# Kernel tuning notes

Measured on AMD Instinct MI355X. Metric: run time of the kernel, lower is better.

The kernel has to match this reference:

```python
import jax, jax.numpy as jnp
import numpy as np

BN_EPS = 1e-5
L2_EPS = 1e-12
TEMP = 0.01


def _fc(x, W, b, gamma, beta, mean, var, normalize):
    # Linear -> ReLU -> BatchNorm1d (eval mode, running stats) [-> L2 normalize]
    y = jnp.maximum(x @ W.T + b, 0.0)
    y = gamma * (y - mean) * jax.lax.rsqrt(var + BN_EPS) + beta
    if normalize:
        n = jnp.linalg.norm(y, axis=-1, keepdims=True)
        y = y / jnp.maximum(n, L2_EPS)
    return y


def setup_inputs() -> dict:
    key = jax.random.key(0)
    B, n, m = 8, 64, 2048
    inp_d0, con_d0, d1, d2, K = 1024, 2048, 2048, 2048, 7
    ks = jax.random.split(key, 16)
    s = 0.02
    inp = {
        'x': jax.random.normal(ks[0], (B, n, inp_d0, K, K), jnp.float32),
        'x_context': jax.random.normal(ks[1], (B, m, con_d0), jnp.float32),
        'num_valid_context_items': jax.random.randint(ks[2], (B, 1), 1, m + 1, jnp.int32),
        'q_W': jax.random.normal(ks[3], (d1, inp_d0)) * s,
        'q_b': jnp.zeros((d1,)),
        'q_gamma': jnp.ones((d1,)),
        'q_beta': jnp.zeros((d1,)),
        'q_mean': jax.random.normal(ks[4], (d1,)) * s,
        'q_var': jax.random.uniform(ks[5], (d1,), minval=0.5, maxval=1.5),
        'k_W': jax.random.normal(ks[6], (d1, con_d0)) * s,
        'k_b': jnp.zeros((d1,)),
        'k_gamma': jnp.ones((d1,)),
        'k_beta': jnp.zeros((d1,)),
        'k_mean': jax.random.normal(ks[7], (d1,)) * s,
        'k_var': jax.random.uniform(ks[8], (d1,), minval=0.5, maxval=1.5),
        'v_W': jax.random.normal(ks[9], (d2, con_d0)) * s,
        'v_b': jnp.zeros((d2,)),
        'v_gamma': jnp.ones((d2,)),
        'v_beta': jnp.zeros((d2,)),
        'v_mean': jax.random.normal(ks[10], (d2,)) * s,
        'v_var': jax.random.uniform(ks[11], (d2,), minval=0.5, maxval=1.5),
        'f_W': jax.random.normal(ks[12], (inp_d0, d2)) * s,
        'f_b': jnp.zeros((inp_d0,)),
        'f_gamma': jnp.ones((inp_d0,)),
        'f_beta': jnp.zeros((inp_d0,)),
        'f_mean': jax.random.normal(ks[13], (inp_d0,)) * s,
        'f_var': jax.random.uniform(ks[14], (inp_d0,), minval=0.5, maxval=1.5),
    }
    return inp


def reference(x, x_context, num_valid_context_items,
              q_W, q_b, q_gamma, q_beta, q_mean, q_var,
              k_W, k_b, k_gamma, k_beta, k_mean, k_var,
              v_W, v_b, v_gamma, v_beta, v_mean, v_var,
              f_W, f_b, f_gamma, f_beta, f_mean, f_var):
    # x: [B, n, D, K, K]; x_context: [B, m, C]; num_valid: [B, 1]
    A_pool = x.mean(axis=(-2, -1))                                  # [B, n, D]
    queries = _fc(A_pool, q_W, q_b, q_gamma, q_beta, q_mean, q_var, True)   # [B, n, d1]
    keys = _fc(x_context, k_W, k_b, k_gamma, k_beta, k_mean, k_var, True)   # [B, m, d1]
    values = _fc(x_context, v_W, v_b, v_gamma, v_beta, v_mean, v_var, True) # [B, m, d2]
    weights = jnp.einsum('bnd,bmd->bnm', queries, keys)             # [B, n, m]
    m = keys.shape[1]
    valid = jnp.arange(m)[None, :] < num_valid_context_items        # [B, m] bool
    weights = jnp.where(valid[:, None, :], weights, -jnp.inf)
    values = values * valid[:, :, None]
    weights = jax.nn.softmax(weights / TEMP, axis=-1)
    wv = jnp.einsum('bnm,bmd->bnd', weights, values)                # [B, n, d2]
    f_context = _fc(wv, f_W, f_b, f_gamma, f_beta, f_mean, f_var, False)    # [B, n, D]
    return x + f_context[..., None, None]
```

## Files before the change

kernel.cpp:

```cpp
#include <hip/hip_runtime.h>

typedef _Float16 f16;
typedef _Float16 f16x8 __attribute__((ext_vector_type(8)));
typedef _Float16 f16x4 __attribute__((ext_vector_type(4)));
typedef float f32x4 __attribute__((ext_vector_type(4)));
typedef float fv4 __attribute__((ext_vector_type(4)));

#define BN_EPS 1e-5f

constexpr int EPI_RAW = 0;
constexpr int EPI_HALF_NORM = 2;
constexpr int EPI_HALF = 3;
constexpr int EPI_BN_F32 = 4;
constexpr int EPI_HALF_NORM_T = 5;

__device__ __forceinline__ void gload_lds16(const void* g, void* l) {
  __builtin_amdgcn_global_load_lds(
      (const __attribute__((address_space(1))) unsigned int*)g,
      (__attribute__((address_space(3))) unsigned int*)l, 16, 0, 0);
}

template <int EPI>
__global__ __launch_bounds__(512, 1) void gemm8_kernel(
    const f16* __restrict__ A, const f16* __restrict__ Bh, int N, int K,
    int gx, f16* __restrict__ Ch, const float* __restrict__ bias,
    const float* __restrict__ gamma, const float* __restrict__ beta,
    const float* __restrict__ mean, const float* __restrict__ var,
    float* __restrict__ norm2) {
  __shared__ __align__(16) char smem[131072];

  const int nwg = gridDim.x;
  const int bid = blockIdx.x;
  const int swz = (bid & 7) * (nwg >> 3) + (bid >> 3);
  const int brow = (swz / gx) * 256;
  const int bcol = (swz % gx) * 256;

  const int tid = threadIdx.x;
  const int lane = tid & 63;
  const int w = tid >> 6;
  const int wm = w >> 2;
  const int wn = w & 3;
  const int l15 = lane & 15;
  const int l4 = lane >> 4;

  const int NT = K >> 6;

  const int c0 = tid ^ ((tid >> 3) & 3);
  const int srow = c0 >> 2;
  const int sk = (c0 & 3) * 8;
  const size_t gA0 = (size_t)(brow + srow) * K + sk;
  const size_t gB0 = (size_t)(bcol + srow) * K + sk;
  const size_t gstep = (size_t)128 * K;
  char* const ldst = smem + tid * 16;

  auto STAGE = [&](int v, int par, int op, int kk) {
    if (v >= NT) return;
    const int k0 = v * 64 + kk * 32;
    const f16* g = (op == 0) ? (A + gA0 + k0) : (Bh + gB0 + k0);
    char* l = ldst + par * 65536 + op * 32768 + kk * 16384;
    gload_lds16(g, l);
    gload_lds16(g + gstep, l + 8192);
  };

  f32x4 acc[8][4] = {};
  f16x8 fb[4];

  const int kx16 = (l4 ^ ((l15 >> 1) & 3)) * 16;
  const int aoff = ((wm * 128 + l15) << 6) + kx16;
  const int boff = 32768 + ((wn * 64 + l15) << 6) + kx16;

  auto ldf = [&](int off) -> f16x8 { return *(const f16x8*)(smem + off); };

  auto PH = [&](int par, int kk, int mi0, bool ldB, int sv, int spar, int sop,
                int skk, int wmode, int tcur, bool bar) {
    const int abase = par * 65536 + kk * 16384;
    if (ldB) {
#pragma unroll
      for (int ni = 0; ni < 4; ++ni) fb[ni] = ldf(abase + boff + (ni << 10));
    }
    f16x8 fa[4];
#pragma unroll
    for (int r = 0; r < 4; ++r) fa[r] = ldf(abase + aoff + ((mi0 + r) << 10));
    STAGE(sv, spar, sop, skk);
    __builtin_amdgcn_s_setprio(1);
#pragma unroll
    for (int r = 0; r < 4; ++r)
#pragma unroll
      for (int ni = 0; ni < 4; ++ni)
        acc[mi0 + r][ni] = __builtin_amdgcn_mfma_f32_16x16x32_f16(
            fa[r], fb[ni], acc[mi0 + r][ni], 0, 0, 0);
    __builtin_amdgcn_s_setprio(0);
    if (wmode == 1) {
      if (tcur + 2 >= NT)
        asm volatile("s_waitcnt vmcnt(0)" ::: "memory");
      else
        asm volatile("s_waitcnt vmcnt(4)" ::: "memory");
    } else if (wmode == 2) {
      if (tcur + 2 < NT) asm volatile("s_waitcnt vmcnt(4)" ::: "memory");
    }
    if (bar) __builtin_amdgcn_s_barrier();
  };

  STAGE(0, 0, 0, 0);
  STAGE(0, 0, 1, 0);
  STAGE(0, 0, 0, 1);
  STAGE(0, 0, 1, 1);
  STAGE(1, 1, 0, 0);
  STAGE(1, 1, 1, 0);
  asm volatile("s_waitcnt vmcnt(4)" ::: "memory");
  __builtin_amdgcn_s_barrier();

  for (int t = 0; t < NT; t += 2) {
    PH(0, 0, 0, true, t + 1, 1, 0, 1, 0, t, false);
    PH(0, 0, 4, false, t + 1, 1, 1, 1, 0, t, true);
    PH(0, 1, 0, true, t + 2, 0, 0, 0, 0, t, false);
    PH(0, 1, 4, false, t + 2, 0, 1, 0, 1, t, true);
    PH(1, 0, 0, true, t + 2, 0, 0, 1, 0, t, false);
    PH(1, 0, 4, false, t + 2, 0, 1, 1, 0, t, true);
    PH(1, 1, 0, true, t + 3, 1, 0, 0, 0, t, false);
    PH(1, 1, 4, false, t + 3, 1, 1, 0, 2, t, true);
  }

  if constexpr (EPI == EPI_HALF_NORM_T) {
    float colsum[4] = {0.f, 0.f, 0.f, 0.f};
#pragma unroll
    for (int mi = 0; mi < 8; ++mi) {
#pragma unroll
      for (int jj = 0; jj < 4; ++jj) {
        const int grow = brow + wm * 128 + mi * 16 + l4 * 4 + jj;
        const float bb = bias[grow], gg = gamma[grow], mm = mean[grow];
        const float vv = var[grow], be = beta[grow];
#pragma unroll
        for (int ni = 0; ni < 4; ++ni) {
          const int gcol = bcol + wn * 64 + ni * 16 + l15;
          float y = fmaxf(acc[mi][ni][jj] + bb, 0.0f);
          y = gg * (y - mm) / sqrtf(vv + BN_EPS) + be;
          Ch[(size_t)grow * N + gcol] = (f16)y;
          colsum[ni] += y * y;
        }
      }
    }
#pragma unroll
    for (int ni = 0; ni < 4; ++ni) {
      float s = colsum[ni];
      s += __shfl_xor(s, 16);
      s += __shfl_xor(s, 32);
      if (l4 == 0)
        atomicAdd(&norm2[bcol + wn * 64 + ni * 16 + l15], s);
    }
  } else {
#pragma unroll
    for (int mi = 0; mi < 8; ++mi) {
#pragma unroll
      for (int jj = 0; jj < 4; ++jj) {
        const int grow = brow + wm * 128 + mi * 16 + l4 * 4 + jj;
        float nsum = 0.0f;
#pragma unroll
        for (int ni = 0; ni < 4; ++ni) {
          const int gcol = bcol + wn * 64 + ni * 16 + l15;
          float y = fmaxf(acc[mi][ni][jj] + bias[gcol], 0.0f);
          y = gamma[gcol] * (y - mean[gcol]) / sqrtf(var[gcol] + BN_EPS) +
              beta[gcol];
          Ch[(size_t)grow * N + gcol] = (f16)y;
          nsum += y * y;
        }
        nsum += __shfl_xor(nsum, 1);
        nsum += __shfl_xor(nsum, 2);
        nsum += __shfl_xor(nsum, 4);
        nsum += __shfl_xor(nsum, 8);
        if (l15 == 0) atomicAdd(&norm2[grow], nsum);
      }
    }
  }
}

template <int BM, int BN, int EPI>
__global__ __launch_bounds__(256, 2) void gemm_kernel(
    const f16* __restrict__ Ah, const f16* __restrict__ Bh, int M, int N,
    int K, long long sAb, long long sBb, long long sCb,
    float* __restrict__ Cf, f16* __restrict__ Ch,
    const float* __restrict__ bias, const float* __restrict__ gamma,
    const float* __restrict__ beta, const float* __restrict__ mean,
    const float* __restrict__ var, float* __restrict__ norm2) {
  (void)M;
  constexpr int BK = 32;
  constexpr int WM = BM / 2, WN = BN / 2;
  constexpr int FM = WM / 16, FN = WN / 16;

  __shared__ __align__(16) f16 lds[(BM + BN) * BK];
  f16* sA = lds;
  f16* sB = lds + BM * BK;

  const int b = blockIdx.z;
  const f16* pA = Ah + (size_t)b * sAb;
  const f16* pB = Bh + (size_t)b * sBb;

  const int brow = blockIdx.y * BM, bcol = blockIdx.x * BN;
  const int t = threadIdx.x, wave = t >> 6, lane = t & 63;
  const int wr = wave >> 1, wc = wave & 1;

  f32x4 acc[FM][FN] = {};

  constexpr int A_CH = BM / 16, B_CH = BN / 16;
  constexpr int TOT = A_CH + B_CH;

  const int srow = lane >> 2;
  const int scol = (lane & 3) * 8;
  const int lr = lane & 15;
  const int lkb = (lane >> 4) * 8;

  for (int k0 = 0; k0 < K; k0 += BK) {
    for (int id = wave; id < TOT; id += 4) {
      const f16* g;
      f16* l;
      if (id < A_CH) {
        g = pA + (size_t)(brow + id * 16 + srow) * K + k0 + scol;
        l = sA + id * 16 * BK;
      } else {
        int c = id - A_CH;
        g = pB + (size_t)(bcol + c * 16 + srow) * K + k0 + scol;
        l = sB + c * 16 * BK;
      }
      gload_lds16(g, l);
    }
    asm volatile("s_waitcnt vmcnt(0)" ::: "memory");
    __syncthreads();

    f16x8 fa[FM], fb[FN];
#pragma unroll
    for (int mi = 0; mi < FM; ++mi)
      fa[mi] = *(const f16x8*)(sA + (size_t)(wr * WM + mi * 16 + lr) * BK + lkb);
#pragma unroll
    for (int ni = 0; ni < FN; ++ni)
      fb[ni] = *(const f16x8*)(sB + (size_t)(wc * WN + ni * 16 + lr) * BK + lkb);
#pragma unroll
    for (int mi = 0; mi < FM; ++mi)
#pragma unroll
      for (int ni = 0; ni < FN; ++ni)
        acc[mi][ni] = __builtin_amdgcn_mfma_f32_16x16x32_f16(fa[mi], fb[ni],
                                                             acc[mi][ni], 0, 0, 0);
    __syncthreads();
  }

#pragma unroll
  for (int mi = 0; mi < FM; ++mi) {
#pragma unroll
    for (int j = 0; j < 4; ++j) {
      const int grow = brow + wr * WM + mi * 16 + (lane >> 4) * 4 + j;
      float nsum = 0.0f;
#pragma unroll
      for (int ni = 0; ni < FN; ++ni) {
        const int gcol = bcol + wc * WN + ni * 16 + lr;
        float val = acc[mi][ni][j];
        if constexpr (EPI == EPI_RAW) {
          Cf[(size_t)b * sCb + (size_t)grow * N + gcol] = val;
        } else if constexpr (EPI == EPI_HALF) {
          Ch[(size_t)b * sCb + (size_t)grow * N + gcol] = (f16)val;
        } else {
          float y = fmaxf(val + bias[gcol], 0.0f);
          y = gamma[gcol] * (y - mean[gcol]) / sqrtf(var[gcol] + BN_EPS) +
              beta[gcol];
          if constexpr (EPI == EPI_BN_F32) {
            Cf[(size_t)grow * N + gcol] = y;
          } else {
            Ch[(size_t)grow * N + gcol] = (f16)y;
            nsum += y * y;
          }
        }
      }
      if constexpr (EPI == EPI_HALF_NORM) {
        nsum += __shfl_xor(nsum, 1);
        nsum += __shfl_xor(nsum, 2);
        nsum += __shfl_xor(nsum, 4);
        nsum += __shfl_xor(nsum, 8);
        if (lr == 0) atomicAdd(&norm2[grow], nsum);
      }
    }
  }
}

__global__ __launch_bounds__(256) void cvt_multi_kernel(
    const float* __restrict__ s0, f16* __restrict__ d0,
    const float* __restrict__ s1, f16* __restrict__ d1,
    const float* __restrict__ s2, f16* __restrict__ d2,
    const float* __restrict__ s3, f16* __restrict__ d3,
    const float* __restrict__ s4, f16* __restrict__ d4, int c0, int c1,
    int c2, int c3, int c4) {
  int i = blockIdx.x * 256 + threadIdx.x;
  if (i >= c4) return;
  const float* s;
  f16* d;
  int j;
  if (i < c0) {
    s = s0; d = d0; j = i;
  } else if (i < c1) {
    s = s1; d = d1; j = i - c0;
  } else if (i < c2) {
    s = s2; d = d2; j = i - c1;
  } else if (i < c3) {
    s = s3; d = d3; j = i - c2;
  } else {
    s = s4; d = d4; j = i - c3;
  }
  fv4 v = ((const fv4*)s)[j];
  f16x4 h;
#pragma unroll
  for (int k = 0; k < 4; ++k) h[k] = (f16)v[k];
  ((f16x4*)d)[j] = h;
}

__global__ __launch_bounds__(256) void pool_kernel(const float* __restrict__ x,
                                                   f16* __restrict__ ah) {
  int bn = blockIdx.x;
  const float* base = x + (size_t)bn * 1024 * 49;
  for (int d = threadIdx.x; d < 1024; d += 256) {
    const float* p = base + (size_t)d * 49;
    float s = 0.f;
#pragma unroll
    for (int j = 0; j < 49; ++j) s += p[j];
    ah[(size_t)bn * 1024 + d] = (f16)(s / 49.0f);
  }
}

__global__ __launch_bounds__(256) void softmax_kernel(
    const float* __restrict__ raw, const float* __restrict__ qn2,
    const float* __restrict__ kn2, const float* __restrict__ vn2,
    const int* __restrict__ nvalid, f16* __restrict__ wgt) {
  const int n = blockIdx.x;
  const int b = blockIdx.y;
  const int row = b * 64 + n;
  const float* r = raw + (size_t)row * 2048;
  const int nv = nvalid[b];
  const float qs = 100.0f / fmaxf(sqrtf(qn2[row]), 1e-12f);

  __shared__ float sl[2048];
  __shared__ float red[4];
  const int t = threadIdx.x;

  float mx = -3.0e38f;
  for (int m = t; m < 2048; m += 256) {
    float v = -3.0e38f;
    if (m < nv) {
      float ks = 1.0f / fmaxf(sqrtf(kn2[b * 2048 + m]), 1e-12f);
      v = r[m] * qs * ks;
    }
    sl[m] = v;
    mx = fmaxf(mx, v);
  }
#pragma unroll
  for (int s = 32; s; s >>= 1) mx = fmaxf(mx, __shfl_xor(mx, s));
  if ((t & 63) == 0) red[t >> 6] = mx;
  __syncthreads();
  mx = fmaxf(fmaxf(red[0], red[1]), fmaxf(red[2], red[3]));
  __syncthreads();

  float sum = 0.f;
  for (int m = t; m < 2048; m += 256) {
    float e = (m < nv) ? __expf(sl[m] - mx) : 0.0f;
    sl[m] = e;
    sum += e;
  }
#pragma unroll
  for (int s = 32; s; s >>= 1) sum += __shfl_xor(sum, s);
  if ((t & 63) == 0) red[t >> 6] = sum;
  __syncthreads();
  sum = red[0] + red[1] + red[2] + red[3];
  const float inv = 1.0f / sum;

  for (int m = t; m < 2048; m += 256) {
    float vs = 1.0f / fmaxf(sqrtf(vn2[b * 2048 + m]), 1e-12f);
    wgt[(size_t)row * 2048 + m] = (f16)(sl[m] * inv * vs);
  }
}

__global__ __launch_bounds__(256) void add_kernel(const float* __restrict__ x,
                                                  const float* __restrict__ fc,
                                                  float* __restrict__ out,
                                                  int n4) {
  int i = blockIdx.x * 256 + threadIdx.x;
  if (i >= n4) return;
  fv4 v = ((const fv4*)x)[i];
  int e = i * 4;
#pragma unroll
  for (int j = 0; j < 4; ++j) v[j] += fc[(e + j) / 49];
  ((fv4*)out)[i] = v;
}

extern "C" void kernel_launch(void* const* d_in, const int* in_sizes, int n_in,
                              void* d_out, int out_size, void* d_ws,
                              size_t ws_size, hipStream_t stream) {
  (void)in_sizes; (void)n_in; (void)out_size; (void)ws_size;
  const float* x = (const float*)d_in[0];
  const float* xc = (const float*)d_in[1];
  const int* nvp = (const int*)d_in[2];
  const float* qW = (const float*)d_in[3];
  const float* qB = (const float*)d_in[4];
  const float* qG = (const float*)d_in[5];
  const float* qBe = (const float*)d_in[6];
  const float* qM = (const float*)d_in[7];
  const float* qV = (const float*)d_in[8];
  const float* kW = (const float*)d_in[9];
  const float* kB = (const float*)d_in[10];
  const float* kG = (const float*)d_in[11];
  const float* kBe = (const float*)d_in[12];
  const float* kM = (const float*)d_in[13];
  const float* kV = (const float*)d_in[14];
  const float* vW = (const float*)d_in[15];
  const float* vB = (const float*)d_in[16];
  const float* vG = (const float*)d_in[17];
  const float* vBe = (const float*)d_in[18];
  const float* vM = (const float*)d_in[19];
  const float* vV = (const float*)d_in[20];
  const float* fW = (const float*)d_in[21];
  const float* fB = (const float*)d_in[22];
  const float* fG = (const float*)d_in[23];
  const float* fBe = (const float*)d_in[24];
  const float* fM = (const float*)d_in[25];
  const float* fV = (const float*)d_in[26];
  float* out = (float*)d_out;

  const int NRq = 512;
  const int NRc = 16384;
  const int Dd = 1024, Cc = 2048, D1 = 2048, D2 = 2048, Mm = 2048;

  char* p = (char*)d_ws;
  auto take = [&](size_t bytes) -> char* {
    char* r = p;
    p += (bytes + 255) & ~(size_t)255;
    return r;
  };
  f16* xch = (f16*)take((size_t)NRc * Cc * 2);
  f16* kh = (f16*)take((size_t)NRc * D1 * 2);
  f16* vT = (f16*)take((size_t)NRc * D2 * 2);
  f16* qWh = (f16*)take((size_t)D1 * Dd * 2);
  f16* kWh = (f16*)take((size_t)D1 * Cc * 2);
  f16* vWh = (f16*)take((size_t)D2 * Cc * 2);
  f16* fWh = (f16*)take((size_t)Dd * D2 * 2);
  f16* Aph = (f16*)take((size_t)NRq * Dd * 2);
  f16* qh = (f16*)take((size_t)NRq * D1 * 2);
  float* norms = (float*)take((size_t)(NRq + 2 * NRc) * 4);
  float* qn2 = norms;
  float* kn2 = norms + NRq;
  float* vn2 = norms + NRq + NRc;
  float* raw = (float*)take((size_t)NRq * Mm * 4);
  f16* wgt = (f16*)take((size_t)NRq * Mm * 2);
  f16* wvh = (f16*)take((size_t)NRq * D2 * 2);
  float* fctx = (float*)take((size_t)NRq * Dd * 4);

  const int n4_0 = NRc * Cc / 4;
  const int n4_1 = D1 * Dd / 4;
  const int n4_2 = D1 * Cc / 4;
  const int n4_3 = D2 * Cc / 4;
  const int n4_4 = Dd * D2 / 4;
  const int cum0 = n4_0, cum1 = cum0 + n4_1, cum2 = cum1 + n4_2,
            cum3 = cum2 + n4_3, cum4 = cum3 + n4_4;
  cvt_multi_kernel<<<dim3((cum4 + 255) / 256), 256, 0, stream>>>(
      xc, xch, qW, qWh, kW, kWh, vW, vWh, fW, fWh, cum0, cum1, cum2, cum3,
      cum4);
  pool_kernel<<<dim3(512), 256, 0, stream>>>(x, Aph);
  hipMemsetAsync(norms, 0, (size_t)(NRq + 2 * NRc) * 4, stream);

  gemm_kernel<32, 128, EPI_HALF_NORM>
      <<<dim3(D1 / 128, NRq / 32, 1), 256, 0, stream>>>(
          Aph, qWh, NRq, D1, Dd, 0, 0, 0, nullptr, qh, qB, qG, qBe, qM, qV,
          qn2);
  gemm8_kernel<EPI_HALF_NORM>
      <<<dim3((NRc / 256) * (D1 / 256)), 512, 0, stream>>>(
          xch, kWh, D1, Cc, D1 / 256, kh, kB, kG, kBe, kM, kV, kn2);
  gemm8_kernel<EPI_HALF_NORM_T>
      <<<dim3((D2 / 256) * (NRc / 256)), 512, 0, stream>>>(
          vWh, xch, NRc, Cc, NRc / 256, vT, vB, vG, vBe, vM, vV, vn2);
  gemm_kernel<32, 128, EPI_RAW><<<dim3(Mm / 128, 2, 8), 256, 0, stream>>>(
      qh, kh, 64, Mm, D1, (long long)64 * D1, (long long)Mm * D1,
      (long long)64 * Mm, raw, nullptr, nullptr, nullptr, nullptr, nullptr,
      nullptr, nullptr);
  softmax_kernel<<<dim3(64, 8), 256, 0, stream>>>(raw, qn2, kn2, vn2, nvp, wgt);
  gemm_kernel<32, 128, EPI_HALF><<<dim3(D2 / 128, 2, 8), 256, 0, stream>>>(
      wgt, vT, 64, D2, Mm, (long long)64 * Mm, (long long)D2 * Mm,
      (long long)64 * D2, nullptr, wvh, nullptr, nullptr, nullptr, nullptr,
      nullptr, nullptr);
  gemm_kernel<32, 128, EPI_BN_F32>
      <<<dim3(Dd / 128, NRq / 32, 1), 256, 0, stream>>>(
          wvh, fWh, NRq, Dd, D2, 0, 0, 0, fctx, nullptr, fB, fG, fBe, fM, fV,
          nullptr);
  add_kernel<<<dim3(25690112 / 4 / 256), 256, 0, stream>>>(x, fctx, out,
                                                           25690112 / 4);
}
```

Before: 585.0 us.

## Software-pipeline LDS fragment loads one phase ahead of MFMAs in GEMM main loop

```diff
diff --git a/kernel.cpp b/kernel.cpp
--- a/kernel.cpp
+++ b/kernel.cpp
@@ -19,6 +19,42 @@
       (const __attribute__((address_space(1))) unsigned int*)g,
       (__attribute__((address_space(3))) unsigned int*)l, 16, 0, 0);
 }
+
+#define LDSA(d0, d1, d2, d3, par, kk, mi0)            \
+  {                                                   \
+    const int ab_ = (par)*65536 + (kk)*16384 + aoff;  \
+    d0 = ldf(ab_ + (((mi0) + 0) << 10));              \
+    d1 = ldf(ab_ + (((mi0) + 1) << 10));              \
+    d2 = ldf(ab_ + (((mi0) + 2) << 10));              \
+    d3 = ldf(ab_ + (((mi0) + 3) << 10));              \
+  }
+#define LDSB(d0, d1, d2, d3, par, kk)                 \
+  {                                                   \
+    const int bb_ = (par)*65536 + (kk)*16384 + boff;  \
+    d0 = ldf(bb_ + (0 << 10));                        \
+    d1 = ldf(bb_ + (1 << 10));                        \
+    d2 = ldf(bb_ + (2 << 10));                        \
+    d3 = ldf(bb_ + (3 << 10));                        \
+  }
+#define MM16(a0, a1, a2, a3, b0, b1, b2, b3, mi0)                              \
+  __builtin_amdgcn_s_setprio(1);                                               \
+  acc[(mi0) + 0][0] = __builtin_amdgcn_mfma_f32_16x16x32_f16(a0, b0, acc[(mi0) + 0][0], 0, 0, 0); \
+  acc[(mi0) + 0][1] = __builtin_amdgcn_mfma_f32_16x16x32_f16(a0, b1, acc[(mi0) + 0][1], 0, 0, 0); \
+  acc[(mi0) + 0][2] = __builtin_amdgcn_mfma_f32_16x16x32_f16(a0, b2, acc[(mi0) + 0][2], 0, 0, 0); \
+  acc[(mi0) + 0][3] = __builtin_amdgcn_mfma_f32_16x16x32_f16(a0, b3, acc[(mi0) + 0][3], 0, 0, 0); \
+  acc[(mi0) + 1][0] = __builtin_amdgcn_mfma_f32_16x16x32_f16(a1, b0, acc[(mi0) + 1][0], 0, 0, 0); \
+  acc[(mi0) + 1][1] = __builtin_amdgcn_mfma_f32_16x16x32_f16(a1, b1, acc[(mi0) + 1][1], 0, 0, 0); \
+  acc[(mi0) + 1][2] = __builtin_amdgcn_mfma_f32_16x16x32_f16(a1, b2, acc[(mi0) + 1][2], 0, 0, 0); \
+  acc[(mi0) + 1][3] = __builtin_amdgcn_mfma_f32_16x16x32_f16(a1, b3, acc[(mi0) + 1][3], 0, 0, 0); \
+  acc[(mi0) + 2][0] = __builtin_amdgcn_mfma_f32_16x16x32_f16(a2, b0, acc[(mi0) + 2][0], 0, 0, 0); \
+  acc[(mi0) + 2][1] = __builtin_amdgcn_mfma_f32_16x16x32_f16(a2, b1, acc[(mi0) + 2][1], 0, 0, 0); \
+  acc[(mi0) + 2][2] = __builtin_amdgcn_mfma_f32_16x16x32_f16(a2, b2, acc[(mi0) + 2][2], 0, 0, 0); \
+  acc[(mi0) + 2][3] = __builtin_amdgcn_mfma_f32_16x16x32_f16(a2, b3, acc[(mi0) + 2][3], 0, 0, 0); \
+  acc[(mi0) + 3][0] = __builtin_amdgcn_mfma_f32_16x16x32_f16(a3, b0, acc[(mi0) + 3][0], 0, 0, 0); \
+  acc[(mi0) + 3][1] = __builtin_amdgcn_mfma_f32_16x16x32_f16(a3, b1, acc[(mi0) + 3][1], 0, 0, 0); \
+  acc[(mi0) + 3][2] = __builtin_amdgcn_mfma_f32_16x16x32_f16(a3, b2, acc[(mi0) + 3][2], 0, 0, 0); \
+  acc[(mi0) + 3][3] = __builtin_amdgcn_mfma_f32_16x16x32_f16(a3, b3, acc[(mi0) + 3][3], 0, 0, 0); \
+  __builtin_amdgcn_s_setprio(0);
 
 template <int EPI>
 __global__ __launch_bounds__(512, 1) void gemm8_kernel(
@@ -63,43 +99,25 @@
   };
 
   f32x4 acc[8][4] = {};
-  f16x8 fb[4];
 
   const int kx16 = (l4 ^ ((l15 >> 1) & 3)) * 16;
   const int aoff = ((wm * 128 + l15) << 6) + kx16;
   const int boff = 32768 + ((wn * 64 + l15) << 6) + kx16;
 
   auto ldf = [&](int off) -> f16x8 { return *(const f16x8*)(smem + off); };
-
-  auto PH = [&](int par, int kk, int mi0, bool ldB, int sv, int spar, int sop,
-                int skk, int wmode, int tcur, bool bar) {
-    const int abase = par * 65536 + kk * 16384;
-    if (ldB) {
-#pragma unroll
-      for (int ni = 0; ni < 4; ++ni) fb[ni] = ldf(abase + boff + (ni << 10));
-    }
-    f16x8 fa[4];
-#pragma unroll
-    for (int r = 0; r < 4; ++r) fa[r] = ldf(abase + aoff + ((mi0 + r) << 10));
-    STAGE(sv, spar, sop, skk);
-    __builtin_amdgcn_s_setprio(1);
-#pragma unroll
-    for (int r = 0; r < 4; ++r)
-#pragma unroll
-      for (int ni = 0; ni < 4; ++ni)
-        acc[mi0 + r][ni] = __builtin_amdgcn_mfma_f32_16x16x32_f16(
-            fa[r], fb[ni], acc[mi0 + r][ni], 0, 0, 0);
-    __builtin_amdgcn_s_setprio(0);
-    if (wmode == 1) {
-      if (tcur + 2 >= NT)
-        asm volatile("s_waitcnt vmcnt(0)" ::: "memory");
-      else
-        asm volatile("s_waitcnt vmcnt(4)" ::: "memory");
-    } else if (wmode == 2) {
-      if (tcur + 2 < NT) asm volatile("s_waitcnt vmcnt(4)" ::: "memory");
-    }
-    if (bar) __builtin_amdgcn_s_barrier();
+  auto BAR = [&]() { __builtin_amdgcn_s_barrier(); };
+  auto VMID = [&](int tcur) {
+    if (tcur + 2 >= NT)
+      asm volatile("s_waitcnt vmcnt(0)" ::: "memory");
+    else
+      asm volatile("s_waitcnt vmcnt(4)" ::: "memory");
   };
+  auto VEND = [&](int tcur) {
+    if (tcur + 2 < NT) asm volatile("s_waitcnt vmcnt(4)" ::: "memory");
+  };
+
+  f16x8 aX0, aX1, aX2, aX3, aY0, aY1, aY2, aY3;
+  f16x8 bX0, bX1, bX2, bX3, bY0, bY1, bY2, bY3;
 
   STAGE(0, 0, 0, 0);
   STAGE(0, 0, 1, 0);
@@ -110,15 +128,48 @@
   asm volatile("s_waitcnt vmcnt(4)" ::: "memory");
   __builtin_amdgcn_s_barrier();
 
+  LDSA(aX0, aX1, aX2, aX3, 0, 0, 0);
+  LDSB(bX0, bX1, bX2, bX3, 0, 0);
+
   for (int t = 0; t < NT; t += 2) {
-    PH(0, 0, 0, true, t + 1, 1, 0, 1, 0, t, false);
-    PH(0, 0, 4, false, t + 1, 1, 1, 1, 0, t, true);
-    PH(0, 1, 0, true, t + 2, 0, 0, 0, 0, t, false);
-    PH(0, 1, 4, false, t + 2, 0, 1, 0, 1, t, true);
-    PH(1, 0, 0, true, t + 2, 0, 0, 1, 0, t, false);
-    PH(1, 0, 4, false, t + 2, 0, 1, 1, 0, t, true);
-    PH(1, 1, 0, true, t + 3, 1, 0, 0, 0, t, false);
-    PH(1, 1, 4, false, t + 3, 1, 1, 0, 2, t, true);
+    STAGE(t + 1, 1, 0, 1);
+    MM16(aX0, aX1, aX2, aX3, bX0, bX1, bX2, bX3, 0);
+    LDSA(aY0, aY1, aY2, aY3, 0, 0, 4);
+    BAR();
+    STAGE(t + 1, 1, 1, 1);
+    MM16(aY0, aY1, aY2, aY3, bX0, bX1, bX2, bX3, 4);
+    LDSA(aX0, aX1, aX2, aX3, 0, 1, 0);
+    LDSB(bY0, bY1, bY2, bY3, 0, 1);
+    BAR();
+    STAGE(t + 2, 0, 0, 0);
+    MM16(aX0, aX1, aX2, aX3, bY0, bY1, bY2, bY3, 0);
+    LDSA(aY0, aY1, aY2, aY3, 0, 1, 4);
+    BAR();
+    STAGE(t + 2, 0, 1, 0);
+    VMID(t);
+    MM16(aY0, aY1, aY2, aY3, bY0, bY1, bY2, bY3, 4);
+    LDSA(aX0, aX1, aX2, aX3, 1, 0, 0);
+    LDSB(bX0, bX1, bX2, bX3, 1, 0);
+    BAR();
+    STAGE(t + 2, 0, 0, 1);
+    MM16(aX0, aX1, aX2, aX3, bX0, bX1, bX2, bX3, 0);
+    LDSA(aY0, aY1, aY2, aY3, 1, 0, 4);
+    BAR();
+    STAGE(t + 2, 0, 1, 1);
+    MM16(aY0, aY1, aY2, aY3, bX0, bX1, bX2, bX3, 4);
+    LDSA(aX0, aX1, aX2, aX3, 1, 1, 0);
+    LDSB(bY0, bY1, bY2, bY3, 1, 1);
+    BAR();
+    STAGE(t + 3, 1, 0, 0);
+    MM16(aX0, aX1, aX2, aX3, bY0, bY1, bY2, bY3, 0);
+    LDSA(aY0, aY1, aY2, aY3, 1, 1, 4);
+    BAR();
+    STAGE(t + 3, 1, 1, 0);
+    VEND(t);
+    MM16(aY0, aY1, aY2, aY3, bY0, bY1, bY2, bY3, 4);
+    LDSA(aX0, aX1, aX2, aX3, 0, 0, 0);
+    LDSB(bX0, bX1, bX2, bX3, 0, 0);
+    BAR();
   }
 
   if constexpr (EPI == EPI_HALF_NORM_T) {
```

New measurement: 584.6 us, median of 2. About the same (-0.1%).

## Split context GEMM tiles across 16 waves with 64x64 per-wave subtiles

Applied to the files above, without the earlier changes.

```diff
diff --git a/kernel.cpp b/kernel.cpp
--- a/kernel.cpp
+++ b/kernel.cpp
@@ -21,7 +21,7 @@
 }
 
 template <int EPI>
-__global__ __launch_bounds__(512, 1) void gemm8_kernel(
+__global__ __launch_bounds__(1024, 4) void gemm16_kernel(
     const f16* __restrict__ A, const f16* __restrict__ Bh, int N, int K,
     int gx, f16* __restrict__ Ch, const float* __restrict__ bias,
     const float* __restrict__ gamma, const float* __restrict__ beta,
@@ -50,84 +50,68 @@
   const int sk = (c0 & 3) * 8;
   const size_t gA0 = (size_t)(brow + srow) * K + sk;
   const size_t gB0 = (size_t)(bcol + srow) * K + sk;
-  const size_t gstep = (size_t)128 * K;
   char* const ldst = smem + tid * 16;
 
-  auto STAGE = [&](int v, int par, int op, int kk) {
+  auto STAGE2 = [&](int v, int par, int kk) {
     if (v >= NT) return;
     const int k0 = v * 64 + kk * 32;
-    const f16* g = (op == 0) ? (A + gA0 + k0) : (Bh + gB0 + k0);
-    char* l = ldst + par * 65536 + op * 32768 + kk * 16384;
-    gload_lds16(g, l);
-    gload_lds16(g + gstep, l + 8192);
+    gload_lds16(A + gA0 + k0, ldst + par * 65536 + kk * 16384);
+    gload_lds16(Bh + gB0 + k0, ldst + par * 65536 + 32768 + kk * 16384);
   };
 
-  f32x4 acc[8][4] = {};
-  f16x8 fb[4];
+  f32x4 acc[4][4] = {};
 
   const int kx16 = (l4 ^ ((l15 >> 1) & 3)) * 16;
-  const int aoff = ((wm * 128 + l15) << 6) + kx16;
+  const int aoff = ((wm * 64 + l15) << 6) + kx16;
   const int boff = 32768 + ((wn * 64 + l15) << 6) + kx16;
 
   auto ldf = [&](int off) -> f16x8 { return *(const f16x8*)(smem + off); };
 
-  auto PH = [&](int par, int kk, int mi0, bool ldB, int sv, int spar, int sop,
-                int skk, int wmode, int tcur, bool bar) {
-    const int abase = par * 65536 + kk * 16384;
-    if (ldB) {
-#pragma unroll
-      for (int ni = 0; ni < 4; ++ni) fb[ni] = ldf(abase + boff + (ni << 10));
-    }
-    f16x8 fa[4];
-#pragma unroll
-    for (int r = 0; r < 4; ++r) fa[r] = ldf(abase + aoff + ((mi0 + r) << 10));
-    STAGE(sv, spar, sop, skk);
+  auto PH = [&](int par, int kk, int sv, int spar, int skk, bool tail) {
+    STAGE2(sv, spar, skk);
+    const int ab = par * 65536 + kk * 16384;
+    f16x8 fa[4], fb[4];
+#pragma unroll
+    for (int i = 0; i < 4; ++i) {
+      fa[i] = ldf(ab + aoff + (i << 10));
+      fb[i] = ldf(ab + boff + (i << 10));
+    }
     __builtin_amdgcn_s_setprio(1);
 #pragma unroll
-    for (int r = 0; r < 4; ++r)
+    for (int mi = 0; mi < 4; ++mi)
 #pragma unroll
       for (int ni = 0; ni < 4; ++ni)
-        acc[mi0 + r][ni] = __builtin_amdgcn_mfma_f32_16x16x32_f16(
-            fa[r], fb[ni], acc[mi0 + r][ni], 0, 0, 0);
+        acc[mi][ni] = __builtin_amdgcn_mfma_f32_16x16x32_f16(
+            fa[mi], fb[ni], acc[mi][ni], 0, 0, 0);
     __builtin_amdgcn_s_setprio(0);
-    if (wmode == 1) {
-      if (tcur + 2 >= NT)
-        asm volatile("s_waitcnt vmcnt(0)" ::: "memory");
-      else
-        asm volatile("s_waitcnt vmcnt(4)" ::: "memory");
-    } else if (wmode == 2) {
-      if (tcur + 2 < NT) asm volatile("s_waitcnt vmcnt(4)" ::: "memory");
-    }
-    if (bar) __builtin_amdgcn_s_barrier();
+    if (tail)
+      asm volatile("s_waitcnt vmcnt(0)" ::: "memory");
+    else
+      asm volatile("s_waitcnt vmcnt(4)" ::: "memory");
+    __builtin_amdgcn_s_barrier();
   };
 
-  STAGE(0, 0, 0, 0);
-  STAGE(0, 0, 1, 0);
-  STAGE(0, 0, 0, 1);
-  STAGE(0, 0, 1, 1);
-  STAGE(1, 1, 0, 0);
-  STAGE(1, 1, 1, 0);
+  STAGE2(0, 0, 0);
+  STAGE2(0, 0, 1);
+  STAGE2(1, 1, 0);
   asm volatile("s_waitcnt vmcnt(4)" ::: "memory");
   __builtin_amdgcn_s_barrier();
 
   for (int t = 0; t < NT; t += 2) {
-    PH(0, 0, 0, true, t + 1, 1, 0, 1, 0, t, false);
-    PH(0, 0, 4, false, t + 1, 1, 1, 1, 0, t, true);
-    PH(0, 1, 0, true, t + 2, 0, 0, 0, 0, t, false);
-    PH(0, 1, 4, false, t + 2, 0, 1, 0, 1, t, true);
-    PH(1, 0, 0, true, t + 2, 0, 0, 1, 0, t, false);
-    PH(1, 0, 4, false, t + 2, 0, 1, 1, 0, t, true);
-    PH(1, 1, 0, true, t + 3, 1, 0, 0, 0, t, false);
-    PH(1, 1, 4, false, t + 3, 1, 1, 0, 2, t, true);
+    const bool tail = (t + 3 >= NT);
+    PH(0, 0, t + 1, 1, 1, tail);
+    PH(0, 1, t + 2, 0, 0, tail);
+    PH(1, 0, t + 2, 0, 1, tail);
+    PH(1, 1, t + 3, 1, 0, tail);
   }
 
   if constexpr (EPI == EPI_HALF_NORM_T) {
     float colsum[4] = {0.f, 0.f, 0.f, 0.f};
 #pragma unroll
-    for (int mi = 0; mi < 8; ++mi) {
+    for (int mi = 0; mi < 4; ++mi) {
 #pragma unroll
       for (int jj = 0; jj < 4; ++jj) {
-        const int grow = brow + wm * 128 + mi * 16 + l4 * 4 + jj;
+        const int grow = brow + wm * 64 + mi * 16 + l4 * 4 + jj;
         const float bb = bias[grow], gg = gamma[grow], mm = mean[grow];
         const float vv = var[grow], be = beta[grow];
 #pragma unroll
@@ -150,10 +134,10 @@
     }
   } else {
 #pragma unroll
-    for (int mi = 0; mi < 8; ++mi) {
+    for (int mi = 0; mi < 4; ++mi) {
 #pragma unroll
       for (int jj = 0; jj < 4; ++jj) {
-        const int grow = brow + wm * 128 + mi * 16 + l4 * 4 + jj;
+        const int grow = brow + wm * 64 + mi * 16 + l4 * 4 + jj;
         float nsum = 0.0f;
 #pragma unroll
         for (int ni = 0; ni < 4; ++ni) {
@@ -464,11 +448,11 @@
       <<<dim3(D1 / 128, NRq / 32, 1), 256, 0, stream>>>(
           Aph, qWh, NRq, D1, Dd, 0, 0, 0, nullptr, qh, qB, qG, qBe, qM, qV,
           qn2);
-  gemm8_kernel<EPI_HALF_NORM>
-      <<<dim3((NRc / 256) * (D1 / 256)), 512, 0, stream>>>(
+  gemm16_kernel<EPI_HALF_NORM>
+      <<<dim3((NRc / 256) * (D1 / 256)), 1024, 0, stream>>>(
           xch, kWh, D1, Cc, D1 / 256, kh, kB, kG, kBe, kM, kV, kn2);
-  gemm8_kernel<EPI_HALF_NORM_T>
-      <<<dim3((D2 / 256) * (NRc / 256)), 512, 0, stream>>>(
+  gemm16_kernel<EPI_HALF_NORM_T>
+      <<<dim3((D2 / 256) * (NRc / 256)), 1024, 0, stream>>>(
           vWh, xch, NRc, Cc, NRc / 256, vT, vB, vG, vBe, vM, vV, vn2);
   gemm_kernel<32, 128, EPI_RAW><<<dim3(Mm / 128, 2, 8), 256, 0, stream>>>(
       qh, kh, 64, Mm, D1, (long long)64 * D1, (long long)Mm * D1,
```

Result: slower. 651.4 us (+11.4%).
